# Kernel optimization log

Measured on AMD Instinct MI355X. Metric: run time of the kernel, lower is better.

## Reference

```python
import jax, jax.numpy as jnp
import numpy as np

B = 4
N0, N1, N2 = 32768, 8192, 2048
C0, C1, C2 = 256, 512, 1024
EPS = 1e-5  # torch BatchNorm1d default eps


def _mlp(x, w1, b1, g, be, w2, b2):
    # Linear -> BatchNorm1d (training-mode batch stats over B and N) -> ReLU -> Linear
    h = x @ w1 + b1                      # (B, N, H)
    mu = jnp.mean(h, axis=(0, 1))
    var = jnp.mean((h - mu) ** 2, axis=(0, 1))  # biased var, as torch BN uses for normalization
    h = jax.nn.relu((h - mu) * jax.lax.rsqrt(var + EPS) * g + be)
    return h @ w2 + b2


def _gather(feats, idx):
    # feats: (B, N_coarse, C), idx: (B, N_fine) -> (B, N_fine, C)
    return jax.vmap(lambda f, i: f[i])(feats, idx)


def _lin(key, fan_in, fan_out, scale=0.02):
    return jax.random.normal(key, (fan_in, fan_out), dtype=jnp.float32) * scale


def setup_inputs() -> dict:
    key = jax.random.key(0)
    ks = jax.random.split(key, 16)
    inp = {
        'f0': jax.random.normal(ks[0], (B, N0, C0), dtype=jnp.float32),
        'f1': jax.random.normal(ks[1], (B, N1, C1), dtype=jnp.float32),
        'f2': jax.random.normal(ks[2], (B, N2, C2), dtype=jnp.float32),
        # up_mlps[0]: MLP(C1, [C1, C0])
        'up0_w1': _lin(ks[3], C1, C1), 'up0_b1': jnp.zeros((C1,), jnp.float32),
        'up0_g': jnp.ones((C1,), jnp.float32), 'up0_be': jnp.zeros((C1,), jnp.float32),
        'up0_w2': _lin(ks[4], C1, C0), 'up0_b2': jnp.zeros((C0,), jnp.float32),
        # up_mlps[1]: MLP(C2, [C2, C1])
        'up1_w1': _lin(ks[5], C2, C2), 'up1_b1': jnp.zeros((C2,), jnp.float32),
        'up1_g': jnp.ones((C2,), jnp.float32), 'up1_be': jnp.zeros((C2,), jnp.float32),
        'up1_w2': _lin(ks[6], C2, C1), 'up1_b2': jnp.zeros((C1,), jnp.float32),
        # skip_mlps[0]: MLP(2*C0, [2*C0, C0])
        'skip0_w1': _lin(ks[7], 2 * C0, 2 * C0), 'skip0_b1': jnp.zeros((2 * C0,), jnp.float32),
        'skip0_g': jnp.ones((2 * C0,), jnp.float32), 'skip0_be': jnp.zeros((2 * C0,), jnp.float32),
        'skip0_w2': _lin(ks[8], 2 * C0, C0), 'skip0_b2': jnp.zeros((C0,), jnp.float32),
        # skip_mlps[1]: MLP(2*C1, [2*C1, C1])
        'skip1_w1': _lin(ks[9], 2 * C1, 2 * C1), 'skip1_b1': jnp.zeros((2 * C1,), jnp.float32),
        'skip1_g': jnp.ones((2 * C1,), jnp.float32), 'skip1_be': jnp.zeros((2 * C1,), jnp.float32),
        'skip1_w2': _lin(ks[10], 2 * C1, C1), 'skip1_b2': jnp.zeros((C1,), jnp.float32),
        'pool0': jax.random.randint(ks[11], (B, N0), 0, N1, dtype=jnp.int32),
        'pool1': jax.random.randint(ks[12], (B, N1), 0, N2, dtype=jnp.int32),
    }
    return inp


def reference(f0, f1, f2,
              up0_w1, up0_b1, up0_g, up0_be, up0_w2, up0_b2,
              up1_w1, up1_b1, up1_g, up1_be, up1_w2, up1_b2,
              skip0_w1, skip0_b1, skip0_g, skip0_be, skip0_w2, skip0_b2,
              skip1_w1, skip1_b1, skip1_g, skip1_be, skip1_w2, skip1_b2,
              pool0, pool1):
    # start at coarsest level
    x = f2                                               # (B, N2, C2)
    # level i = 1
    x = _mlp(x, up1_w1, up1_b1, up1_g, up1_be, up1_w2, up1_b2)   # (B, N2, C1)
    x = _gather(x, pool1)                                 # (B, N1, C1)
    x = _mlp(jnp.concatenate([f1, x], axis=-1),
             skip1_w1, skip1_b1, skip1_g, skip1_be, skip1_w2, skip1_b2)  # (B, N1, C1)
    # level i = 0
    x = _mlp(x, up0_w1, up0_b1, up0_g, up0_be, up0_w2, up0_b2)   # (B, N1, C0)
    x = _gather(x, pool0)                                 # (B, N0, C0)
    x = _mlp(jnp.concatenate([f0, x], axis=-1),
             skip0_w1, skip0_b1, skip0_g, skip0_be, skip0_w2, skip0_b2)  # (B, N0, C0)
    return x
```

## Files before the change

kernel.cpp:

```cpp
#include <hip/hip_runtime.h>


typedef unsigned short u16;
typedef __attribute__((ext_vector_type(8))) short bf16x8;
typedef __attribute__((ext_vector_type(4))) float f32x4;

#define UNROLL _Pragma("unroll")
#define EPW 264

__device__ __forceinline__ float b2f(u16 u) {
    union { unsigned int i; float f; } v; v.i = ((unsigned int)u) << 16; return v.f;
}
__device__ __forceinline__ u16 f2b(float f) {
    union { float f; unsigned int i; } v; v.f = f;
    unsigned int r = v.i + 0x7FFFu + ((v.i >> 16) & 1u);
    return (u16)(r >> 16);
}

__device__ __forceinline__ void gld_lds16(const u16* g, u16* l) {
    __builtin_amdgcn_global_load_lds(
        (const __attribute__((address_space(1))) unsigned int*)g,
        (__attribute__((address_space(3))) unsigned int*)l,
        16, 0, 0);
}

#define VMCNT(n) asm volatile("s_waitcnt vmcnt(" #n ")" ::: "memory")
#define LGKM0    asm volatile("s_waitcnt lgkmcnt(0)" ::: "memory")
#define BAR()    do{ asm volatile("" ::: "memory"); \
                     __builtin_amdgcn_s_barrier(); \
                     asm volatile("" ::: "memory"); }while(0)

union SMem {
    struct { u16 a[2][256 * 64]; u16 b[2][256 * 64]; float ss[2048]; } st;
    u16 ep[256 * EPW];
};

template <bool AFFINE_A, bool STATS, bool OUT_F32, bool GATHER>
__global__ __launch_bounds__(512, 2) void gemm_bn(
    const u16* __restrict__ A, const u16* __restrict__ BT, void* __restrict__ Cout,
    const float* __restrict__ scale, const float* __restrict__ shift,
    const float* __restrict__ bias,
    float* __restrict__ psum, float* __restrict__ psumsq,
    const u16* __restrict__ Xg, const int* __restrict__ pool,
    int nfShift, int Nc, int Chalf,
    int N, int K)
{
    __shared__ __align__(16) SMem sm;

    const int tid  = threadIdx.x;
    const int w    = tid >> 6;
    const int lane = tid & 63;
    const int wm   = w >> 2, wn = w & 3;
    const int l15  = lane & 15;
    const int xorv = (lane & 7) << 3;
    const int swz8 = ((lane & 7) ^ (lane >> 3)) << 3;
    const int kS0  = (((lane >> 4) << 3)) ^ xorv;
    const int kS1  = (32 + ((lane >> 4) << 3)) ^ xorv;

    int bm, bn;
    {
        const int nbn  = (int)gridDim.x;
        const int nwg  = nbn * (int)gridDim.y;
        const int flat = (int)(blockIdx.y * gridDim.x + blockIdx.x);
        const int wg   = (flat & 7) * (nwg >> 3) + (flat >> 3);
        const int lb   = 31 - __builtin_clz(nbn);
        bn = wg & (nbn - 1);
        bm = wg >> lb;
    }

    const u16* aS[2][2]; const u16* xS[2][2]; const u16* bS[2][2];
    int dA[2][2], dB[2][2], wIdx[2][2];
    UNROLL for (int u = 0; u < 2; u++)
    UNROLL for (int ld = 0; ld < 2; ld++) {
        const int urb = w * 16 + ld * 8;
        const int ur  = urb + (lane >> 3);
        {
            const int trb = urb + (urb >= 64 ? 64 : 0) + u * 64;
            const int tr  = ur  + (ur  >= 64 ? 64 : 0) + u * 64;
            dA[u][ld] = trb * 64;
            const int rowG = bm * 256 + tr;
            if constexpr (GATHER) {
                const int b = rowG >> nfShift;
                const int p = pool[rowG];
                aS[u][ld] = A  + (size_t)rowG * Chalf + swz8;
                xS[u][ld] = Xg + ((size_t)b * Nc + p) * Chalf + swz8;
            } else if constexpr (AFFINE_A) {
                aS[u][ld] = A + (size_t)rowG * K + ((lane & 7) << 3);
                wIdx[u][ld] = tr * 64 + swz8;
            } else {
                aS[u][ld] = A + (size_t)rowG * K + swz8;
            }
        }
        {
            const int trb = ((urb >> 5) << 6) + (urb & 31) + u * 32;
            const int tr  = ((ur  >> 5) << 6) + (ur  & 31) + u * 32;
            dB[u][ld] = trb * 64;
            bS[u][ld] = BT + (size_t)(bn * 256 + tr) * K + swz8;
        }
    }

    f32x4 acc[8][4];
    const f32x4 zero = {0.f, 0.f, 0.f, 0.f};
    UNROLL for (int i = 0; i < 8; i++)
    UNROLL for (int j = 0; j < 4; j++) acc[i][j] = zero;
    bf16x8 afr[4][2];
    bf16x8 bfr[2][2][2];
    uint4 rA[2][2];

#define STAGE_A_(u, nb, KOF) do{ \
    if constexpr (AFFINE_A) { \
        rA[u][0] = *(const uint4*)(aS[u][0] + (KOF)); \
        rA[u][1] = *(const uint4*)(aS[u][1] + (KOF)); \
    } else if constexpr (GATHER) { \
        const u16 *s0_, *s1_; \
        if ((KOF) < Chalf) { s0_ = aS[u][0] + (KOF); s1_ = aS[u][1] + (KOF); } \
        else { s0_ = xS[u][0] + ((KOF) - Chalf); s1_ = xS[u][1] + ((KOF) - Chalf); } \
        gld_lds16(s0_, &sm.st.a[(nb)][dA[u][0]]); \
        gld_lds16(s1_, &sm.st.a[(nb)][dA[u][1]]); \
    } else { \
        gld_lds16(aS[u][0] + (KOF), &sm.st.a[(nb)][dA[u][0]]); \
        gld_lds16(aS[u][1] + (KOF), &sm.st.a[(nb)][dA[u][1]]); \
    } }while(0)

#define STAGE_B_(u, nb, KOF) do{ \
    gld_lds16(bS[u][0] + (KOF), &sm.st.b[(nb)][dB[u][0]]); \
    gld_lds16(bS[u][1] + (KOF), &sm.st.b[(nb)][dB[u][1]]); }while(0)

#define AFF_WRITE_(u, tb, KOF) do{ if constexpr (AFFINE_A) { \
    const int kb_ = (KOF) + ((lane & 7) << 3); \
    const float4 sc0_ = *(const float4*)&sm.st.ss[kb_]; \
    const float4 sc1_ = *(const float4*)&sm.st.ss[kb_ + 4]; \
    const float4 sh0_ = *(const float4*)&sm.st.ss[1024 + kb_]; \
    const float4 sh1_ = *(const float4*)&sm.st.ss[1024 + kb_ + 4]; \
    UNROLL for (int ld_ = 0; ld_ < 2; ld_++) { \
        union { uint4 u4; u16 s[8]; } r_, o_; r_.u4 = rA[u][ld_]; \
        o_.s[0] = f2b(fmaxf(b2f(r_.s[0]) * sc0_.x + sh0_.x, 0.f)); \
        o_.s[1] = f2b(fmaxf(b2f(r_.s[1]) * sc0_.y + sh0_.y, 0.f)); \
        o_.s[2] = f2b(fmaxf(b2f(r_.s[2]) * sc0_.z + sh0_.z, 0.f)); \
        o_.s[3] = f2b(fmaxf(b2f(r_.s[3]) * sc0_.w + sh0_.w, 0.f)); \
        o_.s[4] = f2b(fmaxf(b2f(r_.s[4]) * sc1_.x + sh1_.x, 0.f)); \
        o_.s[5] = f2b(fmaxf(b2f(r_.s[5]) * sc1_.y + sh1_.y, 0.f)); \
        o_.s[6] = f2b(fmaxf(b2f(r_.s[6]) * sc1_.z + sh1_.z, 0.f)); \
        o_.s[7] = f2b(fmaxf(b2f(r_.s[7]) * sc1_.w + sh1_.w, 0.f)); \
        *(uint4*)&sm.st.a[(tb)][wIdx[u][ld_]] = o_.u4; } \
    LGKM0; } }while(0)

#define READ_A(buf, qi) do{ const u16* p_ = sm.st.a[(buf)]; \
    UNROLL for (int i_ = 0; i_ < 4; i_++) { \
        const int rb_ = (wm * 128 + ((qi) * 4 + i_) * 16 + l15) * 64; \
        afr[i_][0] = *(const bf16x8*)&p_[rb_ + kS0]; \
        afr[i_][1] = *(const bf16x8*)&p_[rb_ + kS1]; } }while(0)

#define READ_B(buf, qj) do{ const u16* p_ = sm.st.b[(buf)]; \
    UNROLL for (int j_ = 0; j_ < 2; j_++) { \
        const int rb_ = (wn * 64 + ((qj) * 2 + j_) * 16 + l15) * 64; \
        bfr[qj][j_][0] = *(const bf16x8*)&p_[rb_ + kS0]; \
        bfr[qj][j_][1] = *(const bf16x8*)&p_[rb_ + kS1]; } }while(0)

#define MFMA_Q(qi, qj) do{ __builtin_amdgcn_s_setprio(1); \
    UNROLL for (int i_ = 0; i_ < 4; i_++) \
    UNROLL for (int j_ = 0; j_ < 2; j_++) { \
        acc[(qi)*4+i_][(qj)*2+j_] = __builtin_amdgcn_mfma_f32_16x16x32_bf16( \
            afr[i_][0], bfr[qj][j_][0], acc[(qi)*4+i_][(qj)*2+j_], 0, 0, 0); \
        acc[(qi)*4+i_][(qj)*2+j_] = __builtin_amdgcn_mfma_f32_16x16x32_bf16( \
            afr[i_][1], bfr[qj][j_][1], acc[(qi)*4+i_][(qj)*2+j_], 0, 0, 0); } \
    __builtin_amdgcn_s_setprio(0); }while(0)

    const int nkt = K >> 6;

    if constexpr (AFFINE_A) {
        for (int i = tid; i < K; i += 512) {
            sm.st.ss[i] = scale[i]; sm.st.ss[1024 + i] = shift[i];
        }
    }
    STAGE_A_(0, 0, 0); STAGE_B_(0, 0, 0); STAGE_B_(1, 0, 0); STAGE_A_(1, 0, 0);
    asm volatile("s_waitcnt vmcnt(0) lgkmcnt(0)" ::: "memory");
    BAR();
    if constexpr (AFFINE_A) { AFF_WRITE_(0, 0, 0); BAR(); }

    for (int t = 0; t < nkt - 1; ++t) {
        const int buf = t & 1, nb = buf ^ 1;
        const int kofN = (t + 1) << 6;
        STAGE_A_(0, nb, kofN);
        READ_A(buf, 0);
        READ_B(buf, 0);
        BAR();
        MFMA_Q(0, 0);
        STAGE_B_(0, nb, kofN);
        VMCNT(6);
        BAR();
        READ_B(buf, 1);
        MFMA_Q(0, 1);
        STAGE_B_(1, nb, kofN);
        VMCNT(6);
        AFF_WRITE_(1, buf, t << 6);
        BAR();
        READ_A(buf, 1);
        MFMA_Q(1, 1);
        STAGE_A_(1, nb, kofN);
        BAR();
        MFMA_Q(1, 0);
        VMCNT(4);
        AFF_WRITE_(0, nb, kofN);
        BAR();
    }

    {
        const int t = nkt - 1, buf = t & 1;
        READ_A(buf, 0);
        READ_B(buf, 0);
        BAR();
        MFMA_Q(0, 0);
        VMCNT(2);
        BAR();
        READ_B(buf, 1);
        MFMA_Q(0, 1);
        VMCNT(0);
        AFF_WRITE_(1, buf, t << 6);
        BAR();
        READ_A(buf, 1);
        MFMA_Q(1, 1);
        BAR();
        MFMA_Q(1, 0);
    }

    const int cl = l15, quad = lane >> 4;
    if constexpr (OUT_F32) {
        UNROLL for (int j = 0; j < 4; j++) {
            const int col = bn * 256 + wn * 64 + j * 16 + cl;
            const float bcol = bias[col];
            UNROLL for (int i = 0; i < 8; i++) {
                const int r0 = bm * 256 + wm * 128 + i * 16 + quad * 4;
                UNROLL for (int r = 0; r < 4; r++)
                    ((float*)Cout)[(size_t)(r0 + r) * N + col] = acc[i][j][r] + bcol;
            }
        }
    } else {
        UNROLL for (int j = 0; j < 4; j++) {
            const int colL = wn * 64 + j * 16 + cl;
            const int col = bn * 256 + colL;
            float bcol = 0.f;
            if constexpr (!STATS) bcol = bias[col];
            float s = 0.f, ss2 = 0.f;
            UNROLL for (int i = 0; i < 8; i++) {
                const int rL0 = wm * 128 + i * 16 + quad * 4;
                UNROLL for (int r = 0; r < 4; r++) {
                    const float v = acc[i][j][r];
                    if constexpr (STATS) { s += v; ss2 += v * v; }
                    sm.ep[(rL0 + r) * EPW + colL] = f2b(v + bcol);
                }
            }
            if constexpr (STATS) {
                s   += __shfl_xor(s, 16);   s   += __shfl_xor(s, 32);
                ss2 += __shfl_xor(ss2, 16); ss2 += __shfl_xor(ss2, 32);
                if (quad == 0) { atomicAdd(&psum[col], s); atomicAdd(&psumsq[col], ss2); }
            }
        }
        __syncthreads();
        u16* Cb = (u16*)Cout;
        UNROLL for (int it = 0; it < 16; it++) {
            const int row = it * 16 + (tid >> 5);
            const int c8  = (tid & 31) * 8;
            const uint4 v = *(const uint4*)&sm.ep[row * EPW + c8];
            *(uint4*)(Cb + (size_t)(bm * 256 + row) * N + bn * 256 + c8) = v;
        }
    }
#undef STAGE_A_
#undef STAGE_B_
#undef AFF_WRITE_
#undef READ_A
#undef READ_B
#undef MFMA_Q
}

__global__ void cvt_transpose_w(const float* __restrict__ W, u16* __restrict__ WT, int K, int N) {
    __shared__ float t[32][33];
    const int tx = threadIdx.x, ty = threadIdx.y;
    const int n0 = blockIdx.x * 32, k0 = blockIdx.y * 32;
#pragma unroll
    for (int r = 0; r < 4; r++)
        t[ty + r * 8][tx] = W[(size_t)(k0 + ty + r * 8) * N + n0 + tx];
    __syncthreads();
#pragma unroll
    for (int r = 0; r < 4; r++)
        WT[(size_t)(n0 + ty + r * 8) * K + k0 + tx] = f2b(t[tx][ty + r * 8]);
}

__global__ void cvt_f32_bf16(const float* __restrict__ x, u16* __restrict__ y, long n8) {
    const long t = (long)blockIdx.x * 256 + threadIdx.x;
    if (t >= n8) return;
    const float4 a = ((const float4*)x)[t * 2];
    const float4 b = ((const float4*)x)[t * 2 + 1];
    union { uint4 u; u16 s[8]; } o;
    o.s[0] = f2b(a.x); o.s[1] = f2b(a.y); o.s[2] = f2b(a.z); o.s[3] = f2b(a.w);
    o.s[4] = f2b(b.x); o.s[5] = f2b(b.y); o.s[6] = f2b(b.z); o.s[7] = f2b(b.w);
    ((uint4*)y)[t] = o.u;
}

__global__ void bn_finalize(const float* __restrict__ sum, const float* __restrict__ sumsq,
                            const float* __restrict__ g, const float* __restrict__ be,
                            float* __restrict__ scale, float* __restrict__ shift,
                            int Cc, float invM) {
    const int c = blockIdx.x * 256 + threadIdx.x;
    if (c >= Cc) return;
    const float mu = sum[c] * invM;
    const float var = fmaf(sumsq[c], invM, -mu * mu);
    const float sc = g[c] * rsqrtf(var + 1e-5f);
    scale[c] = sc;
    shift[c] = fmaf(-mu, sc, be[c]);
}

extern "C" void kernel_launch(void* const* d_in, const int* in_sizes, int n_in,
                              void* d_out, int out_size, void* d_ws, size_t ws_size,
                              hipStream_t stream) {
    const float* f0     = (const float*)d_in[0];
    const float* f1     = (const float*)d_in[1];
    const float* f2     = (const float*)d_in[2];
    const float* up0_w1 = (const float*)d_in[3];
    const float* up0_g  = (const float*)d_in[5];
    const float* up0_be = (const float*)d_in[6];
    const float* up0_w2 = (const float*)d_in[7];
    const float* up0_b2 = (const float*)d_in[8];
    const float* up1_w1 = (const float*)d_in[9];
    const float* up1_g  = (const float*)d_in[11];
    const float* up1_be = (const float*)d_in[12];
    const float* up1_w2 = (const float*)d_in[13];
    const float* up1_b2 = (const float*)d_in[14];
    const float* sk0_w1 = (const float*)d_in[15];
    const float* sk0_g  = (const float*)d_in[17];
    const float* sk0_be = (const float*)d_in[18];
    const float* sk0_w2 = (const float*)d_in[19];
    const float* sk0_b2 = (const float*)d_in[20];
    const float* sk1_w1 = (const float*)d_in[21];
    const float* sk1_g  = (const float*)d_in[23];
    const float* sk1_be = (const float*)d_in[24];
    const float* sk1_w2 = (const float*)d_in[25];
    const float* sk1_b2 = (const float*)d_in[26];
    const int* pool0    = (const int*)d_in[27];
    const int* pool1    = (const int*)d_in[28];
    float* out = (float*)d_out;

    char* ws = (char*)d_ws;
    size_t off = 0;
    auto alloc = [&](size_t bytes) -> void* {
        void* p = ws + off;
        off += (bytes + 255) & ~(size_t)255;
        return p;
    };
    u16* w_up1_1 = (u16*)alloc((size_t)1024 * 1024 * 2);
    u16* w_up1_2 = (u16*)alloc((size_t)512 * 1024 * 2);
    u16* w_sk1_1 = (u16*)alloc((size_t)1024 * 1024 * 2);
    u16* w_sk1_2 = (u16*)alloc((size_t)512 * 1024 * 2);
    u16* w_up0_1 = (u16*)alloc((size_t)512 * 512 * 2);
    u16* w_up0_2 = (u16*)alloc((size_t)256 * 512 * 2);
    u16* w_sk0_1 = (u16*)alloc((size_t)512 * 512 * 2);
    u16* w_sk0_2 = (u16*)alloc((size_t)256 * 512 * 2);
    float* stats = (float*)alloc((size_t)4 * 4096 * 4);
    u16* Hbuf    = (u16*)alloc((size_t)131072 * 512 * 2);
    u16* Xbuf    = (u16*)alloc((size_t)32768 * 512 * 2);
    u16* f0b     = (u16*)alloc((size_t)4 * 32768 * 256 * 2);
    u16* f1b     = (u16*)alloc((size_t)4 * 8192 * 512 * 2);
    u16* f2b_    = (u16*)alloc((size_t)4 * 2048 * 1024 * 2);

    const dim3 tb(32, 8);
    cvt_transpose_w<<<dim3(32, 32), tb, 0, stream>>>(up1_w1, w_up1_1, 1024, 1024);
    cvt_transpose_w<<<dim3(16, 32), tb, 0, stream>>>(up1_w2, w_up1_2, 1024, 512);
    cvt_transpose_w<<<dim3(32, 32), tb, 0, stream>>>(sk1_w1, w_sk1_1, 1024, 1024);
    cvt_transpose_w<<<dim3(16, 32), tb, 0, stream>>>(sk1_w2, w_sk1_2, 1024, 512);
    cvt_transpose_w<<<dim3(16, 16), tb, 0, stream>>>(up0_w1, w_up0_1, 512, 512);
    cvt_transpose_w<<<dim3(8, 16),  tb, 0, stream>>>(up0_w2, w_up0_2, 512, 256);
    cvt_transpose_w<<<dim3(16, 16), tb, 0, stream>>>(sk0_w1, w_sk0_1, 512, 512);
    cvt_transpose_w<<<dim3(8, 16),  tb, 0, stream>>>(sk0_w2, w_sk0_2, 512, 256);

    hipMemsetAsync(stats, 0, (size_t)4 * 4096 * sizeof(float), stream);
    cvt_f32_bf16<<<4096,  256, 0, stream>>>(f2, f2b_, 8388608L / 8);
    cvt_f32_bf16<<<8192,  256, 0, stream>>>(f1, f1b, 16777216L / 8);
    cvt_f32_bf16<<<16384, 256, 0, stream>>>(f0, f0b, 33554432L / 8);

    float* st0 = stats;
    float* st1 = stats + 4096;
    float* st2 = stats + 8192;
    float* st3 = stats + 12288;

    gemm_bn<false, true, false, false><<<dim3(4, 32), 512, 0, stream>>>(
        f2b_, w_up1_1, Hbuf, nullptr, nullptr, nullptr, st0, st0 + 1024,
        nullptr, nullptr, 0, 0, 0, 1024, 1024);
    bn_finalize<<<4, 256, 0, stream>>>(st0, st0 + 1024, up1_g, up1_be, st0 + 2048, st0 + 3072, 1024, 1.f / 8192.f);
    gemm_bn<true, false, false, false><<<dim3(2, 32), 512, 0, stream>>>(
        Hbuf, w_up1_2, Xbuf, st0 + 2048, st0 + 3072, up1_b2, nullptr, nullptr,
        nullptr, nullptr, 0, 0, 0, 512, 1024);

    gemm_bn<false, true, false, true><<<dim3(4, 128), 512, 0, stream>>>(
        f1b, w_sk1_1, Hbuf, nullptr, nullptr, nullptr, st1, st1 + 1024,
        Xbuf, pool1, 13, 2048, 512, 1024, 1024);
    bn_finalize<<<4, 256, 0, stream>>>(st1, st1 + 1024, sk1_g, sk1_be, st1 + 2048, st1 + 3072, 1024, 1.f / 32768.f);
    gemm_bn<true, false, false, false><<<dim3(2, 128), 512, 0, stream>>>(
        Hbuf, w_sk1_2, Xbuf, st1 + 2048, st1 + 3072, sk1_b2, nullptr, nullptr,
        nullptr, nullptr, 0, 0, 0, 512, 1024);

    gemm_bn<false, true, false, false><<<dim3(2, 128), 512, 0, stream>>>(
        Xbuf, w_up0_1, Hbuf, nullptr, nullptr, nullptr, st2, st2 + 1024,
        nullptr, nullptr, 0, 0, 0, 512, 512);
    bn_finalize<<<2, 256, 0, stream>>>(st2, st2 + 1024, up0_g, up0_be, st2 + 2048, st2 + 3072, 512, 1.f / 32768.f);
    gemm_bn<true, false, false, false><<<dim3(1, 128), 512, 0, stream>>>(
        Hbuf, w_up0_2, Xbuf, st2 + 2048, st2 + 3072, up0_b2, nullptr, nullptr,
        nullptr, nullptr, 0, 0, 0, 256, 512);

    gemm_bn<false, true, false, true><<<dim3(2, 512), 512, 0, stream>>>(
        f0b, w_sk0_1, Hbuf, nullptr, nullptr, nullptr, st3, st3 + 1024,
        Xbuf, pool0, 15, 8192, 256, 512, 512);
    bn_finalize<<<2, 256, 0, stream>>>(st3, st3 + 1024, sk0_g, sk0_be, st3 + 2048, st3 + 3072, 512, 1.f / 131072.f);
    gemm_bn<true, false, true, false><<<dim3(1, 512), 512, 0, stream>>>(
        Hbuf, w_sk0_2, out, st3 + 2048, st3 + 3072, sk0_b2, nullptr, nullptr,
        nullptr, nullptr, 0, 0, 0, 256, 512);
}
```

Baseline: 831.1 us.

## Deepen GEMM A-tile pipeline to triple-buffered LDS with two-step register prefetch

Restructures the bf16 GEMM main loop. For the non-affine paths, A tiles go into a three-slot LDS ring and B into a single buffer, so A loads are issued two k-steps ahead. For the affine (BN+ReLU on A) path, two register sets alternate so global loads for step t+2 overlap the transform and write of step t+1. The goal is to hide global latency behind more MFMA work and to drop some lgkm waits, at the cost of more registers, a manually unrolled-by-two loop, and extra barrier and wait-count complexity that could break occupancy or correctness.

```diff
diff --git a/kernel.cpp b/kernel.cpp
--- a/kernel.cpp
+++ b/kernel.cpp
@@ -31,7 +31,8 @@
                      asm volatile("" ::: "memory"); }while(0)
 
 union SMem {
-    struct { u16 a[2][256 * 64]; u16 b[2][256 * 64]; float ss[2048]; } st;
+    struct { u16 a[3][16384]; u16 b[16384]; } g;
+    struct { u16 a[2][16384]; u16 b[2][16384]; float ss[2048]; } f;
     u16 ep[256 * EPW];
 };
 
@@ -105,35 +106,43 @@
     UNROLL for (int j = 0; j < 4; j++) acc[i][j] = zero;
     bf16x8 afr[4][2];
     bf16x8 bfr[2][2][2];
-    uint4 rA[2][2];
-
-#define STAGE_A_(u, nb, KOF) do{ \
-    if constexpr (AFFINE_A) { \
-        rA[u][0] = *(const uint4*)(aS[u][0] + (KOF)); \
-        rA[u][1] = *(const uint4*)(aS[u][1] + (KOF)); \
-    } else if constexpr (GATHER) { \
+    uint4 rAe[2][2], rAo[2][2];
+
+#define ABASE(T, RS) (AFFINE_A ? &sm.f.a[(T) & 1][0] : &sm.g.a[(RS)][0])
+#define BRD(T)       (AFFINE_A ? &sm.f.b[(T) & 1][0] : &sm.g.b[0])
+#define BSTG(TP)     (AFFINE_A ? &sm.f.b[(TP) & 1][0] : &sm.g.b[0])
+
+#define GLD_B(u, TP, KOF) do{ \
+    u16* bt_ = BSTG(TP); \
+    gld_lds16(bS[u][0] + (KOF), bt_ + dB[u][0]); \
+    gld_lds16(bS[u][1] + (KOF), bt_ + dB[u][1]); }while(0)
+
+#define ISSUE_A(u, WS, KOF) do{ \
+    u16* at_ = &sm.g.a[(WS)][0]; \
+    if constexpr (GATHER) { \
         const u16 *s0_, *s1_; \
         if ((KOF) < Chalf) { s0_ = aS[u][0] + (KOF); s1_ = aS[u][1] + (KOF); } \
         else { s0_ = xS[u][0] + ((KOF) - Chalf); s1_ = xS[u][1] + ((KOF) - Chalf); } \
-        gld_lds16(s0_, &sm.st.a[(nb)][dA[u][0]]); \
-        gld_lds16(s1_, &sm.st.a[(nb)][dA[u][1]]); \
+        gld_lds16(s0_, at_ + dA[u][0]); \
+        gld_lds16(s1_, at_ + dA[u][1]); \
     } else { \
-        gld_lds16(aS[u][0] + (KOF), &sm.st.a[(nb)][dA[u][0]]); \
-        gld_lds16(aS[u][1] + (KOF), &sm.st.a[(nb)][dA[u][1]]); \
+        gld_lds16(aS[u][0] + (KOF), at_ + dA[u][0]); \
+        gld_lds16(aS[u][1] + (KOF), at_ + dA[u][1]); \
     } }while(0)
 
-#define STAGE_B_(u, nb, KOF) do{ \
-    gld_lds16(bS[u][0] + (KOF), &sm.st.b[(nb)][dB[u][0]]); \
-    gld_lds16(bS[u][1] + (KOF), &sm.st.b[(nb)][dB[u][1]]); }while(0)
-
-#define AFF_WRITE_(u, tb, KOF) do{ if constexpr (AFFINE_A) { \
+#define LOAD_RA(SET, u, KOF) do{ \
+    SET[u][0] = *(const uint4*)(aS[u][0] + (KOF)); \
+    SET[u][1] = *(const uint4*)(aS[u][1] + (KOF)); }while(0)
+
+#define AFFW(SET, u, TP, KOF) do{ if constexpr (AFFINE_A) { \
+    u16* at_ = &sm.f.a[(TP) & 1][0]; \
     const int kb_ = (KOF) + ((lane & 7) << 3); \
-    const float4 sc0_ = *(const float4*)&sm.st.ss[kb_]; \
-    const float4 sc1_ = *(const float4*)&sm.st.ss[kb_ + 4]; \
-    const float4 sh0_ = *(const float4*)&sm.st.ss[1024 + kb_]; \
-    const float4 sh1_ = *(const float4*)&sm.st.ss[1024 + kb_ + 4]; \
+    const float4 sc0_ = *(const float4*)&sm.f.ss[kb_]; \
+    const float4 sc1_ = *(const float4*)&sm.f.ss[kb_ + 4]; \
+    const float4 sh0_ = *(const float4*)&sm.f.ss[1024 + kb_]; \
+    const float4 sh1_ = *(const float4*)&sm.f.ss[1024 + kb_ + 4]; \
     UNROLL for (int ld_ = 0; ld_ < 2; ld_++) { \
-        union { uint4 u4; u16 s[8]; } r_, o_; r_.u4 = rA[u][ld_]; \
+        union { uint4 u4; u16 s[8]; } r_, o_; r_.u4 = SET[u][ld_]; \
         o_.s[0] = f2b(fmaxf(b2f(r_.s[0]) * sc0_.x + sh0_.x, 0.f)); \
         o_.s[1] = f2b(fmaxf(b2f(r_.s[1]) * sc0_.y + sh0_.y, 0.f)); \
         o_.s[2] = f2b(fmaxf(b2f(r_.s[2]) * sc0_.z + sh0_.z, 0.f)); \
@@ -142,16 +151,16 @@
         o_.s[5] = f2b(fmaxf(b2f(r_.s[5]) * sc1_.y + sh1_.y, 0.f)); \
         o_.s[6] = f2b(fmaxf(b2f(r_.s[6]) * sc1_.z + sh1_.z, 0.f)); \
         o_.s[7] = f2b(fmaxf(b2f(r_.s[7]) * sc1_.w + sh1_.w, 0.f)); \
-        *(uint4*)&sm.st.a[(tb)][wIdx[u][ld_]] = o_.u4; } \
-    LGKM0; } }while(0)
-
-#define READ_A(buf, qi) do{ const u16* p_ = sm.st.a[(buf)]; \
+        *(uint4*)&at_[wIdx[u][ld_]] = o_.u4; } \
+    } }while(0)
+
+#define READ_A(base, qi) do{ const u16* p_ = (base); \
     UNROLL for (int i_ = 0; i_ < 4; i_++) { \
         const int rb_ = (wm * 128 + ((qi) * 4 + i_) * 16 + l15) * 64; \
         afr[i_][0] = *(const bf16x8*)&p_[rb_ + kS0]; \
         afr[i_][1] = *(const bf16x8*)&p_[rb_ + kS1]; } }while(0)
 
-#define READ_B(buf, qj) do{ const u16* p_ = sm.st.b[(buf)]; \
+#define READ_B(base, qj) do{ const u16* p_ = (base); \
     UNROLL for (int j_ = 0; j_ < 2; j_++) { \
         const int rb_ = (wn * 64 + ((qj) * 2 + j_) * 16 + l15) * 64; \
         bfr[qj][j_][0] = *(const bf16x8*)&p_[rb_ + kS0]; \
@@ -166,62 +175,103 @@
             afr[i_][1], bfr[qj][j_][1], acc[(qi)*4+i_][(qj)*2+j_], 0, 0, 0); } \
     __builtin_amdgcn_s_setprio(0); }while(0)
 
+#define KSTEP(T, RS, WS, SW, SL) do{ \
+    const int kofB_ = ((T) + 1) << 6, kofL_ = ((T) + 2) << 6; \
+    const u16* aR_ = ABASE(T, RS); \
+    const u16* bR_ = BRD(T); \
+     \
+    READ_A(aR_, 0); READ_B(bR_, 0); \
+    if constexpr (!AFFINE_A) LGKM0; \
+    VMCNT(4); BAR(); \
+    GLD_B(0, (T) + 1, kofB_); \
+    MFMA_Q(0, 0); \
+     \
+    READ_B(bR_, 1); \
+    if constexpr (!AFFINE_A) LGKM0; \
+    BAR(); \
+    GLD_B(1, (T) + 1, kofB_); \
+    MFMA_Q(0, 1); \
+     \
+    READ_A(aR_, 1); \
+    if constexpr (AFFINE_A) { AFFW(SW, 0, (T) + 1, kofB_); LOAD_RA(SL, 0, kofL_); } \
+    else { ISSUE_A(0, WS, kofL_); } \
+    BAR(); \
+    MFMA_Q(1, 1); \
+     \
+    if constexpr (AFFINE_A) { AFFW(SW, 1, (T) + 1, kofB_); LOAD_RA(SL, 1, kofL_); LGKM0; } \
+    else { ISSUE_A(1, WS, kofL_); } \
+    MFMA_Q(1, 0); \
+    VMCNT(6); BAR(); \
+}while(0)
+
     const int nkt = K >> 6;
 
     if constexpr (AFFINE_A) {
         for (int i = tid; i < K; i += 512) {
-            sm.st.ss[i] = scale[i]; sm.st.ss[1024 + i] = shift[i];
-        }
-    }
-    STAGE_A_(0, 0, 0); STAGE_B_(0, 0, 0); STAGE_B_(1, 0, 0); STAGE_A_(1, 0, 0);
-    asm volatile("s_waitcnt vmcnt(0) lgkmcnt(0)" ::: "memory");
-    BAR();
-    if constexpr (AFFINE_A) { AFF_WRITE_(0, 0, 0); BAR(); }
-
-    for (int t = 0; t < nkt - 1; ++t) {
-        const int buf = t & 1, nb = buf ^ 1;
-        const int kofN = (t + 1) << 6;
-        STAGE_A_(0, nb, kofN);
-        READ_A(buf, 0);
-        READ_B(buf, 0);
+            sm.f.ss[i] = scale[i]; sm.f.ss[1024 + i] = shift[i];
+        }
+        GLD_B(0, 0, 0); GLD_B(1, 0, 0);
+        LOAD_RA(rAe, 0, 0); LOAD_RA(rAe, 1, 0);
+        LOAD_RA(rAo, 0, 64); LOAD_RA(rAo, 1, 64);
+        LGKM0;
         BAR();
+        AFFW(rAe, 0, 0, 0); AFFW(rAe, 1, 0, 0);
+        LGKM0;
+        BAR();
+    } else {
+        GLD_B(0, 0, 0); GLD_B(1, 0, 0);
+        ISSUE_A(0, 0, 0); ISSUE_A(1, 0, 0);
+        ISSUE_A(0, 1, 64); ISSUE_A(1, 1, 64);
+        VMCNT(0); BAR();
+    }
+
+    int rs = 0;
+    for (int t = 0; t < nkt - 2; t += 2) {
+        const int ws0 = (rs == 0) ? 2 : rs - 1;
+        KSTEP(t, rs, ws0, rAo, rAe);
+        const int rs1 = (rs == 2) ? 0 : rs + 1;
+        const int ws1 = (ws0 == 2) ? 0 : ws0 + 1;
+        KSTEP(t + 1, rs1, ws1, rAe, rAo);
+        rs = (rs1 == 2) ? 0 : rs1 + 1;
+    }
+
+    {
+        const int T = nkt - 2;
+        const int kofB_ = (T + 1) << 6;
+        const u16* aR_ = ABASE(T, rs);
+        const u16* bR_ = BRD(T);
+        READ_A(aR_, 0); READ_B(bR_, 0);
+        if constexpr (!AFFINE_A) LGKM0;
+        VMCNT(4); BAR();
+        GLD_B(0, T + 1, kofB_);
         MFMA_Q(0, 0);
-        STAGE_B_(0, nb, kofN);
-        VMCNT(6);
+        READ_B(bR_, 1);
+        if constexpr (!AFFINE_A) LGKM0;
         BAR();
-        READ_B(buf, 1);
+        GLD_B(1, T + 1, kofB_);
         MFMA_Q(0, 1);
-        STAGE_B_(1, nb, kofN);
-        VMCNT(6);
-        AFF_WRITE_(1, buf, t << 6);
+        READ_A(aR_, 1);
+        if constexpr (AFFINE_A) { AFFW(rAo, 0, T + 1, kofB_); }
         BAR();
-        READ_A(buf, 1);
         MFMA_Q(1, 1);
-        STAGE_A_(1, nb, kofN);
+        if constexpr (AFFINE_A) { AFFW(rAo, 1, T + 1, kofB_); LGKM0; }
+        MFMA_Q(1, 0);
+        VMCNT(2); BAR();
+    }
+    {
+        const int T = nkt - 1;
+        const int rs2 = (rs == 2) ? 0 : rs + 1;
+        const u16* aR_ = ABASE(T, rs2);
+        const u16* bR_ = BRD(T);
+        READ_A(aR_, 0); READ_B(bR_, 0);
+        VMCNT(0); BAR();
+        MFMA_Q(0, 0);
+        READ_B(bR_, 1);
+        MFMA_Q(0, 1);
+        READ_A(aR_, 1);
+        MFMA_Q(1, 1);
+        MFMA_Q(1, 0);
         BAR();
-        MFMA_Q(1, 0);
-        VMCNT(4);
-        AFF_WRITE_(0, nb, kofN);
-        BAR();
-    }
-
-    {
-        const int t = nkt - 1, buf = t & 1;
-        READ_A(buf, 0);
-        READ_B(buf, 0);
-        BAR();
-        MFMA_Q(0, 0);
-        VMCNT(2);
-        BAR();
-        READ_B(buf, 1);
-        MFMA_Q(0, 1);
-        VMCNT(0);
-        AFF_WRITE_(1, buf, t << 6);
-        BAR();
-        READ_A(buf, 1);
-        MFMA_Q(1, 1);
-        BAR();
-        MFMA_Q(1, 0);
     }
 
     const int cl = l15, quad = lane >> 4;
@@ -265,12 +315,17 @@
             *(uint4*)(Cb + (size_t)(bm * 256 + row) * N + bn * 256 + c8) = v;
         }
     }
-#undef STAGE_A_
-#undef STAGE_B_
-#undef AFF_WRITE_
+#undef ABASE
+#undef BRD
+#undef BSTG
+#undef GLD_B
+#undef ISSUE_A
+#undef LOAD_RA
+#undef AFFW
 #undef READ_A
 #undef READ_B
 #undef MFMA_Q
+#undef KSTEP
 }
 
 __global__ void cvt_transpose_w(const float* __restrict__ W, u16* __restrict__ WT, int K, int N) {
```

Measured after the change: 956.2 us. 1.15x slower.

## Triple-buffer A tiles with single-buffered B in non-affine GEMM path

Applied to the files above, without the earlier changes.

Splits the GEMM main loop into two schedules. The affine-A path keeps the existing double buffering. The plain and gather paths now use three A buffers and one B buffer in shared memory, so A loads are issued two K-steps ahead while B is refilled in place between barriers. The goal is to hide global-load latency for the A operand, which can be gathered or streamed, without raising LDS use. The cost is a more complex barrier and vmcnt schedule, with a risk of stalls on the single B buffer.

```diff
diff --git a/kernel.cpp b/kernel.cpp
--- a/kernel.cpp
+++ b/kernel.cpp
@@ -31,7 +31,8 @@
                      asm volatile("" ::: "memory"); }while(0)
 
 union SMem {
-    struct { u16 a[2][256 * 64]; u16 b[2][256 * 64]; float ss[2048]; } st;
+    struct { u16 a[3][16384]; u16 b[16384]; } g;
+    struct { u16 a[2][16384]; u16 b[2][16384]; float ss[2048]; } f;
     u16 ep[256 * EPW];
 };
 
@@ -107,31 +108,35 @@
     bf16x8 bfr[2][2][2];
     uint4 rA[2][2];
 
-#define STAGE_A_(u, nb, KOF) do{ \
-    if constexpr (AFFINE_A) { \
-        rA[u][0] = *(const uint4*)(aS[u][0] + (KOF)); \
-        rA[u][1] = *(const uint4*)(aS[u][1] + (KOF)); \
-    } else if constexpr (GATHER) { \
+#define GLD_B(u, BASE, KOF) do{ \
+    u16* bt_ = (BASE); \
+    gld_lds16(bS[u][0] + (KOF), bt_ + dB[u][0]); \
+    gld_lds16(bS[u][1] + (KOF), bt_ + dB[u][1]); }while(0)
+
+#define ISSUE_A(u, BASE, KOF) do{ \
+    u16* at_ = (BASE); \
+    if constexpr (GATHER) { \
         const u16 *s0_, *s1_; \
         if ((KOF) < Chalf) { s0_ = aS[u][0] + (KOF); s1_ = aS[u][1] + (KOF); } \
         else { s0_ = xS[u][0] + ((KOF) - Chalf); s1_ = xS[u][1] + ((KOF) - Chalf); } \
-        gld_lds16(s0_, &sm.st.a[(nb)][dA[u][0]]); \
-        gld_lds16(s1_, &sm.st.a[(nb)][dA[u][1]]); \
+        gld_lds16(s0_, at_ + dA[u][0]); \
+        gld_lds16(s1_, at_ + dA[u][1]); \
     } else { \
-        gld_lds16(aS[u][0] + (KOF), &sm.st.a[(nb)][dA[u][0]]); \
-        gld_lds16(aS[u][1] + (KOF), &sm.st.a[(nb)][dA[u][1]]); \
+        gld_lds16(aS[u][0] + (KOF), at_ + dA[u][0]); \
+        gld_lds16(aS[u][1] + (KOF), at_ + dA[u][1]); \
     } }while(0)
 
-#define STAGE_B_(u, nb, KOF) do{ \
-    gld_lds16(bS[u][0] + (KOF), &sm.st.b[(nb)][dB[u][0]]); \
-    gld_lds16(bS[u][1] + (KOF), &sm.st.b[(nb)][dB[u][1]]); }while(0)
-
-#define AFF_WRITE_(u, tb, KOF) do{ if constexpr (AFFINE_A) { \
+#define LOAD_RA(u, KOF) do{ \
+    rA[u][0] = *(const uint4*)(aS[u][0] + (KOF)); \
+    rA[u][1] = *(const uint4*)(aS[u][1] + (KOF)); }while(0)
+
+#define AFFW(u, BASE, KOF) do{ if constexpr (AFFINE_A) { \
+    u16* at_ = (BASE); \
     const int kb_ = (KOF) + ((lane & 7) << 3); \
-    const float4 sc0_ = *(const float4*)&sm.st.ss[kb_]; \
-    const float4 sc1_ = *(const float4*)&sm.st.ss[kb_ + 4]; \
-    const float4 sh0_ = *(const float4*)&sm.st.ss[1024 + kb_]; \
-    const float4 sh1_ = *(const float4*)&sm.st.ss[1024 + kb_ + 4]; \
+    const float4 sc0_ = *(const float4*)&sm.f.ss[kb_]; \
+    const float4 sc1_ = *(const float4*)&sm.f.ss[kb_ + 4]; \
+    const float4 sh0_ = *(const float4*)&sm.f.ss[1024 + kb_]; \
+    const float4 sh1_ = *(const float4*)&sm.f.ss[1024 + kb_ + 4]; \
     UNROLL for (int ld_ = 0; ld_ < 2; ld_++) { \
         union { uint4 u4; u16 s[8]; } r_, o_; r_.u4 = rA[u][ld_]; \
         o_.s[0] = f2b(fmaxf(b2f(r_.s[0]) * sc0_.x + sh0_.x, 0.f)); \
@@ -142,16 +147,16 @@
         o_.s[5] = f2b(fmaxf(b2f(r_.s[5]) * sc1_.y + sh1_.y, 0.f)); \
         o_.s[6] = f2b(fmaxf(b2f(r_.s[6]) * sc1_.z + sh1_.z, 0.f)); \
         o_.s[7] = f2b(fmaxf(b2f(r_.s[7]) * sc1_.w + sh1_.w, 0.f)); \
-        *(uint4*)&sm.st.a[(tb)][wIdx[u][ld_]] = o_.u4; } \
+        *(uint4*)&at_[wIdx[u][ld_]] = o_.u4; } \
     LGKM0; } }while(0)
 
-#define READ_A(buf, qi) do{ const u16* p_ = sm.st.a[(buf)]; \
+#define READ_A(base, qi) do{ const u16* p_ = (base); \
     UNROLL for (int i_ = 0; i_ < 4; i_++) { \
         const int rb_ = (wm * 128 + ((qi) * 4 + i_) * 16 + l15) * 64; \
         afr[i_][0] = *(const bf16x8*)&p_[rb_ + kS0]; \
         afr[i_][1] = *(const bf16x8*)&p_[rb_ + kS1]; } }while(0)
 
-#define READ_B(buf, qj) do{ const u16* p_ = sm.st.b[(buf)]; \
+#define READ_B(base, qj) do{ const u16* p_ = (base); \
     UNROLL for (int j_ = 0; j_ < 2; j_++) { \
         const int rb_ = (wn * 64 + ((qj) * 2 + j_) * 16 + l15) * 64; \
         bfr[qj][j_][0] = *(const bf16x8*)&p_[rb_ + kS0]; \
@@ -170,58 +175,119 @@
 
     if constexpr (AFFINE_A) {
         for (int i = tid; i < K; i += 512) {
-            sm.st.ss[i] = scale[i]; sm.st.ss[1024 + i] = shift[i];
-        }
-    }
-    STAGE_A_(0, 0, 0); STAGE_B_(0, 0, 0); STAGE_B_(1, 0, 0); STAGE_A_(1, 0, 0);
-    asm volatile("s_waitcnt vmcnt(0) lgkmcnt(0)" ::: "memory");
-    BAR();
-    if constexpr (AFFINE_A) { AFF_WRITE_(0, 0, 0); BAR(); }
-
-    for (int t = 0; t < nkt - 1; ++t) {
-        const int buf = t & 1, nb = buf ^ 1;
-        const int kofN = (t + 1) << 6;
-        STAGE_A_(0, nb, kofN);
-        READ_A(buf, 0);
-        READ_B(buf, 0);
+            sm.f.ss[i] = scale[i]; sm.f.ss[1024 + i] = shift[i];
+        }
+        LOAD_RA(0, 0);
+        GLD_B(0, &sm.f.b[0][0], 0); GLD_B(1, &sm.f.b[0][0], 0);
+        LOAD_RA(1, 0);
+        asm volatile("s_waitcnt vmcnt(0) lgkmcnt(0)" ::: "memory");
         BAR();
-        MFMA_Q(0, 0);
-        STAGE_B_(0, nb, kofN);
-        VMCNT(6);
+        AFFW(0, &sm.f.a[0][0], 0);
         BAR();
-        READ_B(buf, 1);
-        MFMA_Q(0, 1);
-        STAGE_B_(1, nb, kofN);
-        VMCNT(6);
-        AFF_WRITE_(1, buf, t << 6);
-        BAR();
-        READ_A(buf, 1);
-        MFMA_Q(1, 1);
-        STAGE_A_(1, nb, kofN);
-        BAR();
-        MFMA_Q(1, 0);
-        VMCNT(4);
-        AFF_WRITE_(0, nb, kofN);
-        BAR();
-    }
-
-    {
-        const int t = nkt - 1, buf = t & 1;
-        READ_A(buf, 0);
-        READ_B(buf, 0);
-        BAR();
-        MFMA_Q(0, 0);
-        VMCNT(2);
-        BAR();
-        READ_B(buf, 1);
-        MFMA_Q(0, 1);
-        VMCNT(0);
-        AFF_WRITE_(1, buf, t << 6);
-        BAR();
-        READ_A(buf, 1);
-        MFMA_Q(1, 1);
-        BAR();
-        MFMA_Q(1, 0);
+
+        for (int t = 0; t < nkt - 1; ++t) {
+            const int buf = t & 1, nb = buf ^ 1;
+            const int kofN = (t + 1) << 6;
+            u16* aB = &sm.f.a[buf][0]; u16* aN = &sm.f.a[nb][0];
+            u16* bB = &sm.f.b[buf][0]; u16* bN = &sm.f.b[nb][0];
+            LOAD_RA(0, kofN);
+            READ_A(aB, 0); READ_B(bB, 0);
+            BAR();
+            MFMA_Q(0, 0);
+            GLD_B(0, bN, kofN);
+            VMCNT(6); BAR();
+            READ_B(bB, 1);
+            MFMA_Q(0, 1);
+            GLD_B(1, bN, kofN);
+            VMCNT(6);
+            AFFW(1, aB, t << 6);
+            BAR();
+            READ_A(aB, 1);
+            MFMA_Q(1, 1);
+            LOAD_RA(1, kofN);
+            MFMA_Q(1, 0);
+            VMCNT(4);
+            AFFW(0, aN, kofN);
+            BAR();
+        }
+        {
+            const int t = nkt - 1, buf = t & 1;
+            u16* aB = &sm.f.a[buf][0]; u16* bB = &sm.f.b[buf][0];
+            READ_A(aB, 0); READ_B(bB, 0);
+            BAR();
+            MFMA_Q(0, 0);
+            VMCNT(2); BAR();
+            READ_B(bB, 1);
+            MFMA_Q(0, 1);
+            VMCNT(0);
+            AFFW(1, aB, t << 6);
+            BAR();
+            READ_A(aB, 1);
+            MFMA_Q(1, 1);
+            BAR();
+            MFMA_Q(1, 0);
+        }
+    } else {
+        u16* const bb = &sm.g.b[0];
+        GLD_B(0, bb, 0); GLD_B(1, bb, 0);
+        ISSUE_A(0, &sm.g.a[0][0], 0);  ISSUE_A(1, &sm.g.a[0][0], 0);
+        ISSUE_A(0, &sm.g.a[1][0], 64); ISSUE_A(1, &sm.g.a[1][0], 64);
+        VMCNT(0); BAR();
+
+        int rs = 0;
+        for (int t = 0; t < nkt - 2; ++t) {
+            const int ws = (rs == 0) ? 2 : rs - 1;
+            const int kofB = (t + 1) << 6, kofL = (t + 2) << 6;
+            const u16* aR = &sm.g.a[0][0] + rs * 16384;
+            u16* aW = &sm.g.a[0][0] + ws * 16384;
+            READ_A(aR, 0); READ_B(bb, 0);
+            LGKM0; VMCNT(4); BAR();
+            GLD_B(0, bb, kofB);
+            MFMA_Q(0, 0);
+            READ_B(bb, 1);
+            LGKM0; BAR();
+            GLD_B(1, bb, kofB);
+            MFMA_Q(0, 1);
+            READ_A(aR, 1);
+            ISSUE_A(0, aW, kofL);
+            BAR();
+            MFMA_Q(1, 1);
+            ISSUE_A(1, aW, kofL);
+            MFMA_Q(1, 0);
+            VMCNT(6); BAR();
+            rs = (rs == 2) ? 0 : rs + 1;
+        }
+        {
+            const int t = nkt - 2;
+            const int kofB = (t + 1) << 6;
+            const u16* aR = &sm.g.a[0][0] + rs * 16384;
+            READ_A(aR, 0); READ_B(bb, 0);
+            LGKM0; VMCNT(4); BAR();
+            GLD_B(0, bb, kofB);
+            MFMA_Q(0, 0);
+            READ_B(bb, 1);
+            LGKM0; BAR();
+            GLD_B(1, bb, kofB);
+            MFMA_Q(0, 1);
+            READ_A(aR, 1);
+            BAR();
+            MFMA_Q(1, 1);
+            MFMA_Q(1, 0);
+            VMCNT(2); BAR();
+            rs = (rs == 2) ? 0 : rs + 1;
+        }
+        {
+            const u16* aR = &sm.g.a[0][0] + rs * 16384;
+            READ_A(aR, 0); READ_B(bb, 0);
+            VMCNT(0); BAR();
+            MFMA_Q(0, 0);
+            READ_B(bb, 1);
+            MFMA_Q(0, 1);
+            READ_A(aR, 1);
+            MFMA_Q(1, 1);
+            MFMA_Q(1, 0);
+            LGKM0; BAR();
+        }
     }
 
     const int cl = l15, quad = lane >> 4;
@@ -265,9 +331,10 @@
             *(uint4*)(Cb + (size_t)(bm * 256 + row) * N + bn * 256 + c8) = v;
         }
     }
-#undef STAGE_A_
-#undef STAGE_B_
-#undef AFF_WRITE_
+#undef GLD_B
+#undef ISSUE_A
+#undef LOAD_RA
+#undef AFFW
 #undef READ_A
 #undef READ_B
 #undef MFMA_Q
```

After: 833.4 us. No clear change (+0.3%).
